# Performance work log

Hardware: AMD Instinct MI355X
Metric: run time of the kernel (lower is better)

Reference implementation:

```python
import jax, jax.numpy as jnp
import numpy as np

N = 51200      # total nodes
E = 1638400    # total edges (avg degree 32)
G = 512        # graphs in batch
IN = 16        # input node features
H = 4          # heads
C = 32         # channels per head
HC = H * C     # 128, concat output width
SLOPE = 0.2    # LeakyReLU negative slope
BN_EPS = 1e-5


def _glorot(k, shape, fan):
    return jax.random.normal(k, shape, jnp.float32) / np.sqrt(fan).astype(np.float32)


def setup_inputs() -> dict:
    key = jax.random.key(0)
    ks = jax.random.split(key, 32)
    inp = {}
    inp['x'] = jax.random.normal(ks[0], (N, IN), jnp.float32)
    inp['edge_index'] = jax.random.randint(ks[1], (2, E), 0, N)
    inp['batch'] = jnp.sort(jax.random.randint(ks[2], (N,), 0, G))
    # GATv2 layer 1 (IN -> H*C)
    inp['l1_Wl'] = _glorot(ks[3], (IN, HC), IN)
    inp['l1_bl'] = jnp.zeros((HC,), jnp.float32)
    inp['l1_Wr'] = _glorot(ks[4], (IN, HC), IN)
    inp['l1_br'] = jnp.zeros((HC,), jnp.float32)
    inp['l1_att'] = _glorot(ks[5], (H, C), C)
    inp['l1_bias'] = jnp.zeros((HC,), jnp.float32)
    # GATv2 layer 2 (HC -> H*C)
    inp['l2_Wl'] = _glorot(ks[6], (HC, HC), HC)
    inp['l2_bl'] = jnp.zeros((HC,), jnp.float32)
    inp['l2_Wr'] = _glorot(ks[7], (HC, HC), HC)
    inp['l2_br'] = jnp.zeros((HC,), jnp.float32)
    inp['l2_att'] = _glorot(ks[8], (H, C), C)
    inp['l2_bias'] = jnp.zeros((HC,), jnp.float32)
    # MLP head (HC -> HC -> HC -> 2) with BatchNorm (eval mode, running stats 0/1)
    inp['fc1_W'] = _glorot(ks[9], (HC, HC), HC)
    inp['fc1_b'] = jnp.zeros((HC,), jnp.float32)
    inp['bn1_g'] = jnp.ones((HC,), jnp.float32)
    inp['bn1_b'] = jnp.zeros((HC,), jnp.float32)
    inp['fc2_W'] = _glorot(ks[10], (HC, HC), HC)
    inp['fc2_b'] = jnp.zeros((HC,), jnp.float32)
    inp['bn2_g'] = jnp.ones((HC,), jnp.float32)
    inp['bn2_b'] = jnp.zeros((HC,), jnp.float32)
    inp['fc3_W'] = _glorot(ks[11], (HC, 2), HC)
    inp['fc3_b'] = jnp.zeros((2,), jnp.float32)
    return inp


def gatv2_conv(x, src, dst, Wl, bl, Wr, br, att, bias):
    # PyG GATv2Conv (share_weights=False, concat=True), eval mode (no dropout).
    xl = (x @ Wl + bl).reshape(-1, H, C)  # source transform  [N,H,C]
    xr = (x @ Wr + br).reshape(-1, H, C)  # target transform  [N,H,C]
    e = jax.nn.leaky_relu(xl[src] + xr[dst], SLOPE)   # [E,H,C]
    score = jnp.einsum('ehc,hc->eh', e, att)          # [E,H]
    # segment softmax over edges sharing the same target node
    m = jax.ops.segment_max(score, dst, num_segments=N)
    ex = jnp.exp(score - m[dst])
    denom = jax.ops.segment_sum(ex, dst, num_segments=N)
    alpha = ex / (denom[dst] + 1e-16)                 # [E,H]
    out = jax.ops.segment_sum(xl[src] * alpha[:, :, None], dst, num_segments=N)
    return out.reshape(-1, HC) + bias


def reference(x, edge_index, batch,
              l1_Wl, l1_bl, l1_Wr, l1_br, l1_att, l1_bias,
              l2_Wl, l2_bl, l2_Wr, l2_br, l2_att, l2_bias,
              fc1_W, fc1_b, bn1_g, bn1_b,
              fc2_W, fc2_b, bn2_g, bn2_b,
              fc3_W, fc3_b):
    src, dst = edge_index[0], edge_index[1]
    h = jax.nn.relu(gatv2_conv(x, src, dst, l1_Wl, l1_bl, l1_Wr, l1_br, l1_att, l1_bias))
    h = jax.nn.relu(gatv2_conv(h, src, dst, l2_Wl, l2_bl, l2_Wr, l2_br, l2_att, l2_bias))
    # global mean pool over graphs
    s = jax.ops.segment_sum(h, batch, num_segments=G)
    cnt = jax.ops.segment_sum(jnp.ones((N,), h.dtype), batch, num_segments=G)
    g = s / jnp.maximum(cnt, 1.0)[:, None]            # [G,HC]
    # MLP head; BatchNorm1d in eval mode with running_mean=0, running_var=1
    def bn(z, gamma, beta):
        return z * (gamma / np.sqrt(1.0 + BN_EPS).astype(np.float32)) + beta
    g = jax.nn.relu(bn(g @ fc1_W + fc1_b, bn1_g, bn1_b))
    g = jax.nn.relu(bn(g @ fc2_W + fc2_b, bn2_g, bn2_b))
    return g @ fc3_W + fc3_b                          # [G,2]
```

## Files before the change

kernel.cpp:

```cpp
#include <hip/hip_runtime.h>
#include <math.h>

#define NN 51200
#define EE 1638400
#define GG 512
#define INF 16
#define HCC 128
#define NB 400
#define TILE 4096
#define CSRCAP 4608
#define NBLK (NN / 4)

typedef float vf2 __attribute__((ext_vector_type(2)));
typedef short v8s __attribute__((ext_vector_type(8)));
typedef float v4f __attribute__((ext_vector_type(4)));
#define FMA2 __builtin_elementwise_fma
#define MIN2 __builtin_elementwise_min
#define MAX2 __builtin_elementwise_max


__device__ __forceinline__ int wave_incl_scan(int v, int lane) {
#pragma unroll
    for (int d = 1; d < 64; d <<= 1) {
        int y = __shfl_up(v, d);
        if (lane >= d) v += y;
    }
    return v;
}

__device__ __forceinline__ unsigned short bf16_rtne(float f) {
    unsigned u = __builtin_bit_cast(unsigned, f);
    unsigned r = u + 0x7FFFu + ((u >> 16) & 1u);
    return (unsigned short)(r >> 16);
}

__global__ __launch_bounds__(256) void k_hist(const int* __restrict__ ei,
                                              int* __restrict__ bcnt) {
    __shared__ int h[NB];
    for (int i = threadIdx.x; i < NB; i += 256) h[i] = 0;
    __syncthreads();
    int e0 = blockIdx.x * TILE;
#pragma unroll
    for (int s = 0; s < 16; s++) {
        int d = ei[EE + e0 + s * 256 + threadIdx.x];
        atomicAdd(&h[d >> 7], 1);
    }
    __syncthreads();
    for (int i = threadIdx.x; i < NB; i += 256)
        if (h[i]) atomicAdd(&bcnt[i], h[i]);
}

__global__ __launch_bounds__(512) void k_scan2(const int* __restrict__ bcnt,
                                               int* __restrict__ bbase,
                                               int* __restrict__ gcur,
                                               int* __restrict__ rowptr) {
    __shared__ int sc[512];
    int t = threadIdx.x;
    int v = (t < NB) ? bcnt[t] : 0;
    sc[t] = v;
    __syncthreads();
    for (int off = 1; off < 512; off <<= 1) {
        int u = (t >= off) ? sc[t - off] : 0;
        __syncthreads();
        sc[t] += u;
        __syncthreads();
    }
    if (t < NB) { int ex = sc[t] - v; bbase[t] = ex; gcur[t] = ex; }
    if (t == 0) { bbase[NB] = EE; rowptr[NN] = EE; }
}

__global__ __launch_bounds__(512) void k_binlin1(const int* __restrict__ ei,
                                                 int* __restrict__ gcur,
                                                 unsigned* __restrict__ binned,
                                                 const float* __restrict__ x,
                                                 const float* __restrict__ Wl,
                                                 const float* __restrict__ bl,
                                                 const float* __restrict__ Wr,
                                                 const float* __restrict__ br,
                                                 float* __restrict__ xl,
                                                 float* __restrict__ xr,
                                                 const float* __restrict__ W2l,
                                                 const float* __restrict__ W2r,
                                                 unsigned short* __restrict__ Bhi,
                                                 unsigned short* __restrict__ Blo) {
    __shared__ int h[512];
    __shared__ int lexcl[NB], lcur[NB], baseg[NB];
    __shared__ unsigned stage[TILE];
    __shared__ int wsum[8];
    __shared__ float sx[4][INF];
    int t = threadIdx.x;
    if (blockIdx.x < NB) {
        int lane = t & 63, w = t >> 6;
        h[t] = 0;
        __syncthreads();
        int e0 = blockIdx.x * TILE;
        int sv[8], dv[8];
#pragma unroll
        for (int s = 0; s < 8; s++) {
            int e = e0 + s * 512 + t;
            sv[s] = ei[e];
            dv[s] = ei[EE + e];
            atomicAdd(&h[dv[s] >> 7], 1);
        }
        __syncthreads();
        int myh = h[t];
        int incl = wave_incl_scan(myh, lane);
        if (lane == 63) wsum[w] = incl;
        __syncthreads();
        int woff = 0;
        for (int i = 0; i < w; i++) woff += wsum[i];
        incl += woff;
        if (t < NB) {
            int ex = incl - myh;
            lexcl[t] = ex;
            lcur[t] = ex;
            baseg[t] = atomicAdd(&gcur[t], myh);
        }
        __syncthreads();
#pragma unroll
        for (int s = 0; s < 8; s++) {
            int b = dv[s] >> 7;
            int r = atomicAdd(&lcur[b], 1);
            stage[r] = (unsigned)sv[s] | ((unsigned)dv[s] << 16);
        }
        __syncthreads();
#pragma unroll
        for (int s = 0; s < 8; s++) {
            int idx = s * 512 + t;
            unsigned p = stage[idx];
            int b = (int)(p >> 23);
            binned[baseg[b] + idx - lexcl[b]] = p;
        }
    } else if (blockIdx.x < NB + NN / 4) {
        int bid = blockIdx.x - NB;
        int j = t & 127;
        int ty = t >> 7;
        int row = bid * 4 + ty;
        if (t < 64) {
            sx[t >> 4][t & 15] = x[(size_t)(bid * 4 + (t >> 4)) * INF + (t & 15)];
        }
        __syncthreads();
        float al = bl[j], ar = br[j];
#pragma unroll
        for (int k = 0; k < INF; k++) {
            float xv = sx[ty][k];
            al = fmaf(xv, Wl[k * HCC + j], al);
            ar = fmaf(xv, Wr[k * HCC + j], ar);
        }
        size_t s = ((size_t)(j >> 5) * NN + row) * 32 + (j & 31);
        xl[s] = al;
        xr[s] = ar;
    } else {
        int gt = (blockIdx.x - NB - NN / 4) * 512 + t;
        int ks = gt >> 10;
        int rem = gt & 1023;
        int nt = rem >> 6;
        int lane = rem & 63;
        int n = nt * 16 + (lane & 15);
        int kbase = ks * 32 + (lane >> 4) * 8;
        const float* src = (n < 128) ? (W2l + n) : (W2r + n - 128);
        unsigned short hi8[8], lo8[8];
#pragma unroll
        for (int j = 0; j < 8; j++) {
            float v = src[(size_t)(kbase + j) * HCC];
            unsigned short hb = bf16_rtne(v);
            float hf = __builtin_bit_cast(float, (unsigned)hb << 16);
            hi8[j] = hb;
            lo8[j] = bf16_rtne(v - hf);
        }
        size_t idx = (size_t)gt * 8;
#pragma unroll
        for (int j = 0; j < 8; j++) { Bhi[idx + j] = hi8[j]; Blo[idx + j] = lo8[j]; }
    }
}

__global__ __launch_bounds__(512) void k_csr(const unsigned* __restrict__ binned,
                                             const int* __restrict__ bbase,
                                             int* __restrict__ rowptr,
                                             int* __restrict__ col) {
    int b = blockIdx.x;
    int base = bbase[b];
    int cnt = bbase[b + 1] - base;
    __shared__ int nh[1024], ncur[1024];
    __shared__ unsigned sbin[CSRCAP];
    __shared__ int wsum[8];
    int t = threadIdx.x;
    int lane = t & 63, w = t >> 6;
    nh[t] = 0;
    nh[t + 512] = 0;
    __syncthreads();
    for (int e = t; e < cnt; e += 512) {
        unsigned p = binned[base + e];
        if (e < CSRCAP) sbin[e] = p;
        unsigned src = p & 0xFFFFu;
        int key = (int)(((p >> 16) & 127u) << 3) | (int)(src >> 13);
        atomicAdd(&nh[key], 1);
    }
    __syncthreads();
    int c0 = nh[2 * t], c1 = nh[2 * t + 1];
    int tot = c0 + c1;
    int incl = wave_incl_scan(tot, lane);
    if (lane == 63) wsum[w] = incl;
    __syncthreads();
    int woff = 0;
    for (int i = 0; i < w; i++) woff += wsum[i];
    int tex = incl + woff - tot;
    ncur[2 * t] = base + tex;
    ncur[2 * t + 1] = base + tex + c0;
    if ((t & 3) == 0) rowptr[(b << 7) + (t >> 2)] = base + tex;
    __syncthreads();
    for (int e = t; e < cnt; e += 512) {
        unsigned p = (e < CSRCAP) ? sbin[e] : binned[base + e];
        unsigned src = p & 0xFFFFu;
        int key = (int)(((p >> 16) & 127u) << 3) | (int)(src >> 13);
        int r = atomicAdd(&ncur[key], 1);
        col[r] = (int)src;
    }
}

__global__ __launch_bounds__(256) void k_lin2(const float* __restrict__ hin,
                                              const unsigned short* __restrict__ Bhi,
                                              const unsigned short* __restrict__ Blo,
                                              const float* __restrict__ bl,
                                              const float* __restrict__ br,
                                              float* __restrict__ outl,
                                              float* __restrict__ outr) {
    const int tid = threadIdx.x;
    const int wv = tid >> 6;
    const int lane = tid & 63;
    const int m = lane & 15;
    const int quad = lane >> 4;
    const int r0 = blockIdx.x * 64 + wv * 16;
    const float* arow = hin + (size_t)(r0 + m) * HCC + quad * 8;
    const v8s* bh = (const v8s*)Bhi;
    const v8s* bo = (const v8s*)Blo;

    v4f acc[16];
#pragma unroll
    for (int nt = 0; nt < 16; nt++) acc[nt] = (v4f){0.f, 0.f, 0.f, 0.f};

#pragma unroll
    for (int ks = 0; ks < 4; ks++) {
        const float4 av0 = *(const float4*)(arow + ks * 32);
        const float4 av1 = *(const float4*)(arow + ks * 32 + 4);
        const float af[8] = {av0.x, av0.y, av0.z, av0.w, av1.x, av1.y, av1.z, av1.w};
        v8s ahi, alo;
#pragma unroll
        for (int e = 0; e < 8; e++) {
            unsigned short hb = bf16_rtne(af[e]);
            float hf = __builtin_bit_cast(float, (unsigned)hb << 16);
            ahi[e] = (short)hb;
            alo[e] = (short)bf16_rtne(af[e] - hf);
        }
        const int base = ks * 16 * 64 + lane;
#pragma unroll
        for (int nt = 0; nt < 16; nt++) {
            v8s bhv = bh[base + nt * 64];
            v8s blv = bo[base + nt * 64];
            acc[nt] = __builtin_amdgcn_mfma_f32_16x16x32_bf16(ahi, bhv, acc[nt], 0, 0, 0);
            acc[nt] = __builtin_amdgcn_mfma_f32_16x16x32_bf16(ahi, blv, acc[nt], 0, 0, 0);
            acc[nt] = __builtin_amdgcn_mfma_f32_16x16x32_bf16(alo, bhv, acc[nt], 0, 0, 0);
        }
    }
#pragma unroll
    for (int nt = 0; nt < 16; nt++) {
        int n = nt * 16 + m;
        int c = n & 127;
        float bv = (n < 128) ? bl[c] : br[c];
        float* outp = ((n < 128) ? outl : outr) + (size_t)(c >> 5) * NN * 32 + (c & 31);
#pragma unroll
        for (int r = 0; r < 4; r++) {
            int row = r0 + quad * 4 + r;
            outp[(size_t)row * 32] = acc[nt][r] + bv;
        }
    }
}

__global__ __launch_bounds__(256) void k_attn(const int* __restrict__ rowptr,
                                              const int* __restrict__ col,
                                              const float* __restrict__ xl,
                                              const float* __restrict__ xr,
                                              const float* __restrict__ att,
                                              const float* __restrict__ bias,
                                              float* __restrict__ hout) {
    const int wave = threadIdx.x >> 6;
    const int lane = threadIdx.x & 63;
    const int sub = lane >> 3;
    const int hl = (lane >> 2) & 1;
    const int hq = lane & 3;
    const int pair = blockIdx.x / NBLK;
    const int n = (blockIdx.x - pair * NBLK) * 4 + wave;
    const int head = 2 * pair + hl;

    const float* xlh = xl + (size_t)head * NN * 32;
    const float* xrp = xr + ((size_t)head * NN + n) * 32 + hq * 8;
    const float4 xrv0 = *(const float4*)(xrp);
    const float4 xrv1 = *(const float4*)(xrp + 4);
    const float4 at0 = *(const float4*)(att + head * 32 + hq * 8);
    const float4 at1 = *(const float4*)(att + head * 32 + hq * 8 + 4);
    const vf2 xr01 = {xrv0.x, xrv0.y}, xr23 = {xrv0.z, xrv0.w};
    const vf2 xr45 = {xrv1.x, xrv1.y}, xr67 = {xrv1.z, xrv1.w};
    const vf2 at01 = {at0.x, at0.y}, at23 = {at0.z, at0.w};
    const vf2 at45 = {at1.x, at1.y}, at67 = {at1.z, at1.w};
    const vf2 Z2 = {0.f, 0.f}, C2 = {0.2f, 0.2f};
    const unsigned choff = (unsigned)hq * 32u;

    const int base = rowptr[n];
    const int deg = rowptr[n + 1] - base;

    float m = -INFINITY, l = 0.f;
    vf2 a01 = Z2, a23 = Z2, a45 = Z2, a67 = Z2;

    for (int i0 = 0; i0 < deg; i0 += 64) {
        int mye = 0;
        if (i0 + lane < deg) mye = col[base + i0 + lane];
        const int cnt = min(64, deg - i0);
        const int events = (cnt + 15) >> 4;
        for (int g = 0; g < events; ++g) {
            float4 v0[2], v1[2];
            float p[2];
#pragma unroll
            for (int k = 0; k < 2; ++k) {
                const int src = __shfl(mye, 16 * g + 8 * k + sub);
                const unsigned voff = ((unsigned)src << 7) + choff;
                v0[k] = *(const float4*)((const char*)xlh + voff);
                v1[k] = *(const float4*)((const char*)xlh + voff + 16);
            }
#pragma unroll
            for (int k = 0; k < 2; ++k) {
                const vf2 v01 = {v0[k].x, v0[k].y}, v23 = {v0[k].z, v0[k].w};
                const vf2 v45 = {v1[k].x, v1[k].y}, v67 = {v1[k].z, v1[k].w};
                vf2 e, kk, p2;
                e = v01 + xr01; kk = FMA2(C2, MIN2(e, Z2), MAX2(e, Z2)); p2 = kk * at01;
                e = v23 + xr23; kk = FMA2(C2, MIN2(e, Z2), MAX2(e, Z2)); p2 = FMA2(kk, at23, p2);
                e = v45 + xr45; kk = FMA2(C2, MIN2(e, Z2), MAX2(e, Z2)); p2 = FMA2(kk, at45, p2);
                e = v67 + xr67; kk = FMA2(C2, MIN2(e, Z2), MAX2(e, Z2)); p2 = FMA2(kk, at67, p2);
                float pp = p2.x + p2.y;
                pp += __shfl_xor(pp, 1);
                pp += __shfl_xor(pp, 2);
                if ((16 * g + 8 * k + sub) >= cnt) pp = -INFINITY;
                p[k] = pp;
            }
            float pm = fmaxf(p[0], p[1]);
            pm = fmaxf(pm, __shfl_xor(pm, 8));
            pm = fmaxf(pm, __shfl_xor(pm, 16));
            pm = fmaxf(pm, __shfl_xor(pm, 32));
            const float mn = fmaxf(m, pm);
            const float sc = __expf(m - mn);
            const float w0 = __expf(p[0] - mn);
            const float w1 = __expf(p[1] - mn);
            l = fmaf(l, sc, w0 + w1);
            const vf2 S = {sc, sc}, W0 = {w0, w0}, W1 = {w1, w1};
            const vf2 u01 = {v0[0].x, v0[0].y}, u23 = {v0[0].z, v0[0].w};
            const vf2 u45 = {v1[0].x, v1[0].y}, u67 = {v1[0].z, v1[0].w};
            const vf2 t01 = {v0[1].x, v0[1].y}, t23 = {v0[1].z, v0[1].w};
            const vf2 t45 = {v1[1].x, v1[1].y}, t67 = {v1[1].z, v1[1].w};
            a01 = FMA2(W1, t01, FMA2(W0, u01, a01 * S));
            a23 = FMA2(W1, t23, FMA2(W0, u23, a23 * S));
            a45 = FMA2(W1, t45, FMA2(W0, u45, a45 * S));
            a67 = FMA2(W1, t67, FMA2(W0, u67, a67 * S));
            m = mn;
        }
    }
    l += __shfl_xor(l, 8);
    l += __shfl_xor(l, 16);
    l += __shfl_xor(l, 32);
    float af[8] = {a01.x, a01.y, a23.x, a23.y, a45.x, a45.y, a67.x, a67.y};
#pragma unroll
    for (int i = 0; i < 8; i++) {
        af[i] += __shfl_xor(af[i], 8);
        af[i] += __shfl_xor(af[i], 16);
        af[i] += __shfl_xor(af[i], 32);
    }
    const float inv = 1.f / (l + 1e-16f);
    if (sub == 0) {
        const float4 b0 = *(const float4*)(bias + head * 32 + hq * 8);
        const float4 b1 = *(const float4*)(bias + head * 32 + hq * 8 + 4);
        float4 o0, o1;
        o0.x = fmaxf(fmaf(af[0], inv, b0.x), 0.f);
        o0.y = fmaxf(fmaf(af[1], inv, b0.y), 0.f);
        o0.z = fmaxf(fmaf(af[2], inv, b0.z), 0.f);
        o0.w = fmaxf(fmaf(af[3], inv, b0.w), 0.f);
        o1.x = fmaxf(fmaf(af[4], inv, b1.x), 0.f);
        o1.y = fmaxf(fmaf(af[5], inv, b1.y), 0.f);
        o1.z = fmaxf(fmaf(af[6], inv, b1.z), 0.f);
        o1.w = fmaxf(fmaf(af[7], inv, b1.w), 0.f);
        float* hp = hout + (size_t)n * HCC + head * 32 + hq * 8;
        *(float4*)(hp) = o0;
        *(float4*)(hp + 4) = o1;
    }
}

__global__ __launch_bounds__(128) void k_head(const float* __restrict__ h,
                                              const int* __restrict__ batch,
                                              const float* __restrict__ fc1W, const float* __restrict__ fc1b,
                                              const float* __restrict__ bn1g, const float* __restrict__ bn1b,
                                              const float* __restrict__ fc2W, const float* __restrict__ fc2b,
                                              const float* __restrict__ bn2g, const float* __restrict__ bn2b,
                                              const float* __restrict__ fc3W, const float* __restrict__ fc3b,
                                              float* __restrict__ out) {
    int g = blockIdx.x;
    int j = threadIdx.x;
    __shared__ float buf[HCC], buf2[HCC];
    int lo = 0, hi = NN;
    while (lo < hi) { int mid = (lo + hi) >> 1; if (batch[mid] < g) lo = mid + 1; else hi = mid; }
    int s = lo;
    lo = 0; hi = NN;
    while (lo < hi) { int mid = (lo + hi) >> 1; if (batch[mid] < g + 1) lo = mid + 1; else hi = mid; }
    int e = lo;
    float s0 = 0.f, s1 = 0.f, s2 = 0.f, s3 = 0.f;
    int n = s;
    for (; n + 3 < e; n += 4) {
        s0 += h[(size_t)n * HCC + j];
        s1 += h[(size_t)(n + 1) * HCC + j];
        s2 += h[(size_t)(n + 2) * HCC + j];
        s3 += h[(size_t)(n + 3) * HCC + j];
    }
    for (; n < e; n++) s0 += h[(size_t)n * HCC + j];
    float sum = (s0 + s1) + (s2 + s3);
    float cnt = (float)(e - s);
    buf[j] = sum / fmaxf(cnt, 1.0f);
    __syncthreads();
    const float SQ = 1.00000499998749994f;
    float a = fc1b[j];
    for (int k = 0; k < HCC; k++) a = fmaf(buf[k], fc1W[k * HCC + j], a);
    a = fmaf(a, bn1g[j] / SQ, bn1b[j]);
    a = fmaxf(a, 0.f);
    buf2[j] = a;
    __syncthreads();
    a = fc2b[j];
    for (int k = 0; k < HCC; k++) a = fmaf(buf2[k], fc2W[k * HCC + j], a);
    a = fmaf(a, bn2g[j] / SQ, bn2b[j]);
    a = fmaxf(a, 0.f);
    buf[j] = a;
    __syncthreads();
    if (j < 2) {
        float o = fc3b[j];
        for (int k = 0; k < HCC; k++) o = fmaf(buf[k], fc3W[k * 2 + j], o);
        out[g * 2 + j] = o;
    }
}

extern "C" void kernel_launch(void* const* d_in, const int* in_sizes, int n_in,
                              void* d_out, int out_size, void* d_ws, size_t ws_size,
                              hipStream_t stream) {
    const float* x      = (const float*)d_in[0];
    const int*   ei     = (const int*)d_in[1];
    const int*   batch  = (const int*)d_in[2];
    const float* l1_Wl  = (const float*)d_in[3];
    const float* l1_bl  = (const float*)d_in[4];
    const float* l1_Wr  = (const float*)d_in[5];
    const float* l1_br  = (const float*)d_in[6];
    const float* l1_att = (const float*)d_in[7];
    const float* l1_bias= (const float*)d_in[8];
    const float* l2_Wl  = (const float*)d_in[9];
    const float* l2_bl  = (const float*)d_in[10];
    const float* l2_Wr  = (const float*)d_in[11];
    const float* l2_br  = (const float*)d_in[12];
    const float* l2_att = (const float*)d_in[13];
    const float* l2_bias= (const float*)d_in[14];
    const float* fc1_W  = (const float*)d_in[15];
    const float* fc1_b  = (const float*)d_in[16];
    const float* bn1_g  = (const float*)d_in[17];
    const float* bn1_b  = (const float*)d_in[18];
    const float* fc2_W  = (const float*)d_in[19];
    const float* fc2_b  = (const float*)d_in[20];
    const float* bn2_g  = (const float*)d_in[21];
    const float* bn2_b  = (const float*)d_in[22];
    const float* fc3_W  = (const float*)d_in[23];
    const float* fc3_b  = (const float*)d_in[24];
    float* out = (float*)d_out;

    float* xl = (float*)d_ws;
    float* xr = xl + (size_t)NN * HCC;
    float* h  = xr + (size_t)NN * HCC;
    int* rowptr = (int*)(h + (size_t)NN * HCC);
    int* col    = rowptr + (NN + 1);
    int* bcnt   = col + EE;
    int* bbase  = bcnt + NB;
    int* gcur   = bbase + (NB + 1);
    uintptr_t bp = ((uintptr_t)(gcur + NB) + 15) & ~(uintptr_t)15;
    unsigned short* Bhi = (unsigned short*)bp;
    unsigned short* Blo = Bhi + 32768;
    unsigned* binned = (unsigned*)h;

    hipMemsetAsync(bcnt, 0, NB * sizeof(int), stream);
    k_hist<<<EE / TILE, 256, 0, stream>>>(ei, bcnt);
    k_scan2<<<1, 512, 0, stream>>>(bcnt, bbase, gcur, rowptr);
    k_binlin1<<<NB + NN / 4 + 8, 512, 0, stream>>>(ei, gcur, binned,
                                                   x, l1_Wl, l1_bl, l1_Wr, l1_br, xl, xr,
                                                   l2_Wl, l2_Wr, Bhi, Blo);
    k_csr<<<NB, 512, 0, stream>>>(binned, bbase, rowptr, col);

    k_attn<<<2 * NBLK, 256, 0, stream>>>(rowptr, col, xl, xr, l1_att, l1_bias, h);

    k_lin2<<<NN / 64, 256, 0, stream>>>(h, Bhi, Blo, l2_bl, l2_br, xl, xr);
    k_attn<<<2 * NBLK, 256, 0, stream>>>(rowptr, col, xl, xr, l2_att, l2_bias, h);

    k_head<<<GG, 128, 0, stream>>>(h, batch, fc1_W, fc1_b, bn1_g, bn1_b,
                                   fc2_W, fc2_b, bn2_g, bn2_b, fc3_W, fc3_b, out);
}
```

Measured before the change: 442.0 us.

## Fuse histogram with layer-1 linear and split binning into its own kernel

The histogram pass now runs in the same launch as the layer-1 node linear transform and the weight bf16 split, so those independent tasks share one grid. The edge binning moves into a separate kernel with half-size tiles (2048 edges) and twice as many blocks, each thread scanning two bucket counts. This is meant to overlap the histogram with the linear work and to spread binning over more blocks with less shared memory each. In exchange, edge indices are read once more in a separate launch and there are more global atomics on the bucket cursors.

```diff
diff --git a/kernel.cpp b/kernel.cpp
--- a/kernel.cpp
+++ b/kernel.cpp
@@ -8,6 +8,7 @@
 #define HCC 128
 #define NB 400
 #define TILE 4096
+#define TILEB 2048
 #define CSRCAP 4608
 #define NBLK (NN / 4)
 
@@ -34,103 +35,33 @@
     return (unsigned short)(r >> 16);
 }
 
-__global__ __launch_bounds__(256) void k_hist(const int* __restrict__ ei,
-                                              int* __restrict__ bcnt) {
+__global__ __launch_bounds__(512) void k_histlin1(const int* __restrict__ ei,
+                                                  int* __restrict__ bcnt,
+                                                  const float* __restrict__ x,
+                                                  const float* __restrict__ Wl,
+                                                  const float* __restrict__ bl,
+                                                  const float* __restrict__ Wr,
+                                                  const float* __restrict__ br,
+                                                  float* __restrict__ xl,
+                                                  float* __restrict__ xr,
+                                                  const float* __restrict__ W2l,
+                                                  const float* __restrict__ W2r,
+                                                  unsigned short* __restrict__ Bhi,
+                                                  unsigned short* __restrict__ Blo) {
     __shared__ int h[NB];
-    for (int i = threadIdx.x; i < NB; i += 256) h[i] = 0;
-    __syncthreads();
-    int e0 = blockIdx.x * TILE;
-#pragma unroll
-    for (int s = 0; s < 16; s++) {
-        int d = ei[EE + e0 + s * 256 + threadIdx.x];
-        atomicAdd(&h[d >> 7], 1);
-    }
-    __syncthreads();
-    for (int i = threadIdx.x; i < NB; i += 256)
-        if (h[i]) atomicAdd(&bcnt[i], h[i]);
-}
-
-__global__ __launch_bounds__(512) void k_scan2(const int* __restrict__ bcnt,
-                                               int* __restrict__ bbase,
-                                               int* __restrict__ gcur,
-                                               int* __restrict__ rowptr) {
-    __shared__ int sc[512];
-    int t = threadIdx.x;
-    int v = (t < NB) ? bcnt[t] : 0;
-    sc[t] = v;
-    __syncthreads();
-    for (int off = 1; off < 512; off <<= 1) {
-        int u = (t >= off) ? sc[t - off] : 0;
-        __syncthreads();
-        sc[t] += u;
-        __syncthreads();
-    }
-    if (t < NB) { int ex = sc[t] - v; bbase[t] = ex; gcur[t] = ex; }
-    if (t == 0) { bbase[NB] = EE; rowptr[NN] = EE; }
-}
-
-__global__ __launch_bounds__(512) void k_binlin1(const int* __restrict__ ei,
-                                                 int* __restrict__ gcur,
-                                                 unsigned* __restrict__ binned,
-                                                 const float* __restrict__ x,
-                                                 const float* __restrict__ Wl,
-                                                 const float* __restrict__ bl,
-                                                 const float* __restrict__ Wr,
-                                                 const float* __restrict__ br,
-                                                 float* __restrict__ xl,
-                                                 float* __restrict__ xr,
-                                                 const float* __restrict__ W2l,
-                                                 const float* __restrict__ W2r,
-                                                 unsigned short* __restrict__ Bhi,
-                                                 unsigned short* __restrict__ Blo) {
-    __shared__ int h[512];
-    __shared__ int lexcl[NB], lcur[NB], baseg[NB];
-    __shared__ unsigned stage[TILE];
-    __shared__ int wsum[8];
     __shared__ float sx[4][INF];
     int t = threadIdx.x;
     if (blockIdx.x < NB) {
-        int lane = t & 63, w = t >> 6;
-        h[t] = 0;
+        if (t < NB) h[t] = 0;
         __syncthreads();
         int e0 = blockIdx.x * TILE;
-        int sv[8], dv[8];
 #pragma unroll
         for (int s = 0; s < 8; s++) {
-            int e = e0 + s * 512 + t;
-            sv[s] = ei[e];
-            dv[s] = ei[EE + e];
-            atomicAdd(&h[dv[s] >> 7], 1);
+            int d = ei[EE + e0 + s * 512 + t];
+            atomicAdd(&h[d >> 7], 1);
         }
         __syncthreads();
-        int myh = h[t];
-        int incl = wave_incl_scan(myh, lane);
-        if (lane == 63) wsum[w] = incl;
-        __syncthreads();
-        int woff = 0;
-        for (int i = 0; i < w; i++) woff += wsum[i];
-        incl += woff;
-        if (t < NB) {
-            int ex = incl - myh;
-            lexcl[t] = ex;
-            lcur[t] = ex;
-            baseg[t] = atomicAdd(&gcur[t], myh);
-        }
-        __syncthreads();
-#pragma unroll
-        for (int s = 0; s < 8; s++) {
-            int b = dv[s] >> 7;
-            int r = atomicAdd(&lcur[b], 1);
-            stage[r] = (unsigned)sv[s] | ((unsigned)dv[s] << 16);
-        }
-        __syncthreads();
-#pragma unroll
-        for (int s = 0; s < 8; s++) {
-            int idx = s * 512 + t;
-            unsigned p = stage[idx];
-            int b = (int)(p >> 23);
-            binned[baseg[b] + idx - lexcl[b]] = p;
-        }
+        if (t < NB && h[t]) atomicAdd(&bcnt[t], h[t]);
     } else if (blockIdx.x < NB + NN / 4) {
         int bid = blockIdx.x - NB;
         int j = t & 127;
@@ -171,6 +102,77 @@
         size_t idx = (size_t)gt * 8;
 #pragma unroll
         for (int j = 0; j < 8; j++) { Bhi[idx + j] = hi8[j]; Blo[idx + j] = lo8[j]; }
+    }
+}
+
+__global__ __launch_bounds__(512) void k_scan2(const int* __restrict__ bcnt,
+                                               int* __restrict__ bbase,
+                                               int* __restrict__ gcur,
+                                               int* __restrict__ rowptr) {
+    __shared__ int sc[512];
+    int t = threadIdx.x;
+    int v = (t < NB) ? bcnt[t] : 0;
+    sc[t] = v;
+    __syncthreads();
+    for (int off = 1; off < 512; off <<= 1) {
+        int u = (t >= off) ? sc[t - off] : 0;
+        __syncthreads();
+        sc[t] += u;
+        __syncthreads();
+    }
+    if (t < NB) { int ex = sc[t] - v; bbase[t] = ex; gcur[t] = ex; }
+    if (t == 0) { bbase[NB] = EE; rowptr[NN] = EE; }
+}
+
+__global__ __launch_bounds__(512) void k_bin(const int* __restrict__ ei,
+                                             int* __restrict__ gcur,
+                                             unsigned* __restrict__ binned) {
+    __shared__ int hh[NB], lexcl[NB], lcur[NB], baseg[NB];
+    __shared__ unsigned stage[TILEB];
+    __shared__ int wsum[8];
+    int t = threadIdx.x;
+    int lane = t & 63, w = t >> 6;
+    if (t < NB) hh[t] = 0;
+    __syncthreads();
+    int e0 = blockIdx.x * TILEB;
+    int sv[4], dv[4];
+#pragma unroll
+    for (int s = 0; s < 4; s++) {
+        int e = e0 + s * 512 + t;
+        sv[s] = ei[e];
+        dv[s] = ei[EE + e];
+        atomicAdd(&hh[dv[s] >> 7], 1);
+    }
+    __syncthreads();
+    int c0 = 0, c1 = 0;
+    if (t < NB / 2) { c0 = hh[2 * t]; c1 = hh[2 * t + 1]; }
+    int tot = c0 + c1;
+    int incl = wave_incl_scan(tot, lane);
+    if (lane == 63) wsum[w] = incl;
+    __syncthreads();
+    int woff = 0;
+    for (int i = 0; i < w; i++) woff += wsum[i];
+    int ex = incl + woff - tot;
+    if (t < NB / 2) {
+        lexcl[2 * t] = ex;          lcur[2 * t] = ex;
+        lexcl[2 * t + 1] = ex + c0; lcur[2 * t + 1] = ex + c0;
+        baseg[2 * t] = atomicAdd(&gcur[2 * t], c0);
+        baseg[2 * t + 1] = atomicAdd(&gcur[2 * t + 1], c1);
+    }
+    __syncthreads();
+#pragma unroll
+    for (int s = 0; s < 4; s++) {
+        int b = dv[s] >> 7;
+        int r = atomicAdd(&lcur[b], 1);
+        stage[r] = (unsigned)sv[s] | ((unsigned)dv[s] << 16);
+    }
+    __syncthreads();
+#pragma unroll
+    for (int s = 0; s < 4; s++) {
+        int idx = s * 512 + t;
+        unsigned p = stage[idx];
+        int b = (int)(p >> 23);
+        binned[baseg[b] + idx - lexcl[b]] = p;
     }
 }
 
@@ -485,11 +487,11 @@
     unsigned* binned = (unsigned*)h;
 
     hipMemsetAsync(bcnt, 0, NB * sizeof(int), stream);
-    k_hist<<<EE / TILE, 256, 0, stream>>>(ei, bcnt);
+    k_histlin1<<<NB + NN / 4 + 8, 512, 0, stream>>>(ei, bcnt,
+                                                    x, l1_Wl, l1_bl, l1_Wr, l1_br, xl, xr,
+                                                    l2_Wl, l2_Wr, Bhi, Blo);
     k_scan2<<<1, 512, 0, stream>>>(bcnt, bbase, gcur, rowptr);
-    k_binlin1<<<NB + NN / 4 + 8, 512, 0, stream>>>(ei, gcur, binned,
-                                                   x, l1_Wl, l1_bl, l1_Wr, l1_br, xl, xr,
-                                                   l2_Wl, l2_Wr, Bhi, Blo);
+    k_bin<<<EE / TILEB, 512, 0, stream>>>(ei, gcur, binned);
     k_csr<<<NB, 512, 0, stream>>>(binned, bbase, rowptr, col);
 
     k_attn<<<2 * NBLK, 256, 0, stream>>>(rowptr, col, xl, xr, l1_att, l1_bias, h);
```

After: 476.0 us. 7.7% more time.
